# Optimization experiments

Measured on AMD Instinct MI355X. Metric: run time of the kernel, lower is better.

## Reference

```python
import jax, jax.numpy as jnp
import numpy as np

B, N_INST, H, W = 8, 64, 480, 480
EPS = 1e-12  # torch F.normalize eps


def setup_inputs() -> dict:
    key = jax.random.key(0)
    k1, k2, k3, k4, k5, k6 = jax.random.split(key, 6)
    # binary instance masks (output of connected-component labeling in the original)
    instance_masks = (jax.random.uniform(k1, (N_INST, H, W)) < 0.3).astype(jnp.float32)
    sample_ids = jax.random.randint(k2, (N_INST,), 0, B, dtype=jnp.int64)
    quaternion = jax.random.normal(k3, (B, 4, H, W), dtype=jnp.float32)
    scales = jax.random.normal(k4, (B, 3, H, W), dtype=jnp.float32)
    xy = jax.random.normal(k5, (B, 2, H, W), dtype=jnp.float32)
    z = jax.random.normal(k6, (B, H, W), dtype=jnp.float32)
    return {"instance_masks": instance_masks, "sample_ids": sample_ids,
            "quaternion": quaternion, "scales": scales, "xy": xy, "z": z}


def reference(instance_masks, sample_ids, quaternion, scales, xy, z):
    # instance_masks: [N,H,W] binary float; sample_ids: [N] in [0,B)
    mask_size = jnp.sum(instance_masks, axis=(-2, -1))  # [N]

    def masked_mean(d):  # d: [N,C,H,W] -> [N,C]
        return jnp.einsum('nhw,nchw->nc', instance_masks, d) / mask_size[:, None]

    # quaternion: masked mean then L2-normalize along channel dim
    q_agg = masked_mean(quaternion[sample_ids])                       # [N,4]
    q_agg = q_agg / jnp.maximum(jnp.linalg.norm(q_agg, axis=1, keepdims=True), EPS)
    # scales: masked mean
    s_agg = masked_mean(scales[sample_ids])                           # [N,3]
    # z: masked mean of [N,1,H,W] then exp
    z_agg = jnp.exp(masked_mean(z[sample_ids][:, None]))              # [N,1]
    # xy: masked dense map (passed on to hough voting downstream)
    xy_masked = instance_masks[:, None] * xy[sample_ids]              # [N,2,H,W]
    return q_agg, s_agg, z_agg, xy_masked
```

## Files before the change

### kernel.cpp

```cpp
#include <hip/hip_runtime.h>
#include <math.h>

#define HW      (480 * 480)
#define HW4     (HW / 4)
#define NINST   64
#define NB      8
#define NV      9
#define GI      8
#define ITER    3
#define NBLK    75
#define THREADS 256

typedef float f4 __attribute__((ext_vector_type(4)));

__device__ __forceinline__ float dot4(const float4 a, const float4 b) {
    return (a.x * b.x + a.y * b.y) + (a.z * b.z + a.w * b.w);
}

template <int CTRL>
__device__ __forceinline__ float dpp_add(float x) {
    int s = __builtin_amdgcn_update_dpp(0, __float_as_int(x), CTRL, 0xf, 0xf, false);
    return x + __int_as_float(s);
}
__device__ __forceinline__ float wave_sum(float x) {
    x = dpp_add<0x111>(x);
    x = dpp_add<0x112>(x);
    x = dpp_add<0x114>(x);
    x = dpp_add<0x118>(x);
    x = dpp_add<0x142>(x);
    x = dpp_add<0x143>(x);
    return x;
}

__global__ __launch_bounds__(THREADS, 2) void agg_main(
    const float* __restrict__ masks,
    const int*   __restrict__ sids,
    const float* __restrict__ quat,
    const float* __restrict__ scales,
    const float* __restrict__ xy,
    const float* __restrict__ z,
    float*       __restrict__ out,
    float*       __restrict__ part)
{
    const int tid = threadIdx.x;
    const int bx  = blockIdx.x;
    const int b   = blockIdx.y;

    __shared__ int   ilist[NINST];
    __shared__ int   scnt;
    __shared__ float swred[4][GI * NV];

    if (tid < 64) {
        const bool mine = (sids[tid] == b);
        const unsigned long long mk = __ballot(mine);
        if (mine) {
            const int rank = __popcll(mk & ((1ull << tid) - 1ull));
            ilist[rank] = tid;
        }
        if (tid == 0) scnt = __popcll(mk);
    }
    __syncthreads();
    const int cnt = scnt;

    const float4* M  = (const float4*)masks;
    const float4* Q  = (const float4*)quat   + (size_t)b * 4 * HW4;
    const float4* S  = (const float4*)scales + (size_t)b * 3 * HW4;
    const float4* X  = (const float4*)xy     + (size_t)b * 2 * HW4;
    const float4* Zp = (const float4*)z      + (size_t)b * HW4;
    f4*           O  = (f4*)(out + 512);

    const int lane = tid & 63;
    const int wid  = tid >> 6;

    for (int g0 = 0; g0 < cnt; g0 += GI) {
        int  nidx[GI];
        bool valid[GI];
#pragma unroll
        for (int j = 0; j < GI; ++j) {
            valid[j] = (g0 + j < cnt);
            nidx[j]  = ilist[valid[j] ? (g0 + j) : (cnt - 1)];
        }

        float acc[GI][NV];
#pragma unroll
        for (int j = 0; j < GI; ++j)
#pragma unroll
            for (int v = 0; v < NV; ++v) acc[j][v] = 0.0f;

#pragma unroll
        for (int it = 0; it < ITER; ++it) {
            const int i = (bx * ITER + it) * THREADS + tid;

            float4 m[GI];
#pragma unroll
            for (int j = 0; j < GI; ++j)
                m[j] = M[(size_t)nidx[j] * HW4 + i];
            const float4 vq0 = Q[0 * HW4 + i];
            const float4 vq1 = Q[1 * HW4 + i];
            const float4 vq2 = Q[2 * HW4 + i];
            const float4 vq3 = Q[3 * HW4 + i];
            const float4 vs0 = S[0 * HW4 + i];
            const float4 vs1 = S[1 * HW4 + i];
            const float4 vs2 = S[2 * HW4 + i];
            const float4 vx0 = X[0 * HW4 + i];
            const float4 vx1 = X[1 * HW4 + i];
            const float4 vz  = Zp[i];

#pragma unroll
            for (int j = 0; j < GI; ++j) {
                if (valid[j]) {
                    f4 o0 = { m[j].x * vx0.x, m[j].y * vx0.y,
                              m[j].z * vx0.z, m[j].w * vx0.w };
                    f4 o1 = { m[j].x * vx1.x, m[j].y * vx1.y,
                              m[j].z * vx1.z, m[j].w * vx1.w };
                    __builtin_nontemporal_store(o0, &O[((size_t)nidx[j] * 2 + 0) * HW4 + i]);
                    __builtin_nontemporal_store(o1, &O[((size_t)nidx[j] * 2 + 1) * HW4 + i]);
                }
            }

#pragma unroll
            for (int j = 0; j < GI; ++j) {
                acc[j][0] += (m[j].x + m[j].y) + (m[j].z + m[j].w);
                acc[j][1] += dot4(m[j], vq0);
                acc[j][2] += dot4(m[j], vq1);
                acc[j][3] += dot4(m[j], vq2);
                acc[j][4] += dot4(m[j], vq3);
                acc[j][5] += dot4(m[j], vs0);
                acc[j][6] += dot4(m[j], vs1);
                acc[j][7] += dot4(m[j], vs2);
                acc[j][8] += dot4(m[j], vz);
            }
        }

#pragma unroll
        for (int j = 0; j < GI; ++j)
#pragma unroll
            for (int v = 0; v < NV; ++v) {
                const float t = wave_sum(acc[j][v]);
                if (lane == 63) swred[wid][j * NV + v] = t;
            }
        __syncthreads();
        if (tid < GI * NV) {
            const int j = tid / NV;
            const int v = tid - j * NV;
            if (g0 + j < cnt) {
                const int n = ilist[g0 + j];
                part[((size_t)n * NBLK + bx) * NV + v] =
                    (swred[0][tid] + swred[1][tid]) + (swred[2][tid] + swred[3][tid]);
            }
        }
        __syncthreads();
    }
}

__global__ __launch_bounds__(THREADS) void agg_final(
    const float* __restrict__ part,
    float*       __restrict__ out)
{
    const int n   = blockIdx.x;
    const int tid = threadIdx.x;

    float vals[NV];
#pragma unroll
    for (int v = 0; v < NV; ++v) vals[v] = 0.0f;
    for (int c = tid; c < NBLK; c += THREADS) {
        const float* p = part + ((size_t)n * NBLK + c) * NV;
#pragma unroll
        for (int v = 0; v < NV; ++v) vals[v] += p[v];
    }

    __shared__ float sred[4][NV];
    const int lane = tid & 63;
    const int wid  = tid >> 6;
#pragma unroll
    for (int v = 0; v < NV; ++v) {
        float x = vals[v];
#pragma unroll
        for (int off = 32; off > 0; off >>= 1)
            x += __shfl_down(x, off, 64);
        if (lane == 0) sred[wid][v] = x;
    }
    __syncthreads();

    if (tid == 0) {
        float s[NV];
#pragma unroll
        for (int v = 0; v < NV; ++v)
            s[v] = (sred[0][v] + sred[1][v]) + (sred[2][v] + sred[3][v]);

        const float inv = 1.0f / s[0];
        const float q0 = s[1] * inv, q1 = s[2] * inv, q2 = s[3] * inv, q3 = s[4] * inv;
        const float norm = sqrtf(q0 * q0 + q1 * q1 + q2 * q2 + q3 * q3);
        const float d = fmaxf(norm, 1e-12f);
        out[n * 4 + 0] = q0 / d;
        out[n * 4 + 1] = q1 / d;
        out[n * 4 + 2] = q2 / d;
        out[n * 4 + 3] = q3 / d;

        out[256 + n * 3 + 0] = s[5] * inv;
        out[256 + n * 3 + 1] = s[6] * inv;
        out[256 + n * 3 + 2] = s[7] * inv;

        out[448 + n] = expf(s[8] * inv);
    }
}

extern "C" void kernel_launch(void* const* d_in, const int* in_sizes, int n_in,
                              void* d_out, int out_size, void* d_ws, size_t ws_size,
                              hipStream_t stream) {
    const float* masks  = (const float*)d_in[0];
    const int*   sids   = (const int*)d_in[1];
    const float* quat   = (const float*)d_in[2];
    const float* scales = (const float*)d_in[3];
    const float* xy     = (const float*)d_in[4];
    const float* z      = (const float*)d_in[5];
    float* out  = (float*)d_out;
    float* part = (float*)d_ws;

    dim3 grid(NBLK, NB);
    agg_main<<<grid, THREADS, 0, stream>>>(masks, sids, quat, scales, xy, z, out, part);
    agg_final<<<NINST, THREADS, 0, stream>>>(part, out);
}
```

Baseline: 253.1 us.

## Sort instances by batch and assign blocks to balanced instance groups

Each block now owns one group of four instances from a single batch. Blocks find their group from an in-kernel counting sort of sample ids and stride over the pixels, replacing the old scheme where each batch block serially walked all of its instances in groups of eight. The aim is to remove the load imbalance from uneven instance counts per batch and to raise occupancy by using smaller per-thread accumulators and a higher launch bound. The cost is that the dense quaternion, scale, xy and z maps are re-read by more groups. Some grid rows also exit early and do no work.

```diff
diff --git a/kernel.cpp b/kernel.cpp
--- a/kernel.cpp
+++ b/kernel.cpp
@@ -1,14 +1,13 @@
 #include <hip/hip_runtime.h>
 #include <math.h>
 
-#define HW      (480 * 480)
-#define HW4     (HW / 4)
+#define HW4     57600
 #define NINST   64
 #define NB      8
 #define NV      9
-#define GI      8
-#define ITER    3
-#define NBLK    75
+#define GI      4
+#define NQMAX   22
+#define NBLKX   90
 #define THREADS 256
 
 typedef float f4 __attribute__((ext_vector_type(4)));
@@ -32,7 +31,7 @@
     return x;
 }
 
-__global__ __launch_bounds__(THREADS, 2) void agg_main(
+__global__ __launch_bounds__(THREADS, 4) void agg_main(
     const float* __restrict__ masks,
     const int*   __restrict__ sids,
     const float* __restrict__ quat,
@@ -44,23 +43,49 @@
 {
     const int tid = threadIdx.x;
     const int bx  = blockIdx.x;
-    const int b   = blockIdx.y;
-
-    __shared__ int   ilist[NINST];
-    __shared__ int   scnt;
+    const int q   = blockIdx.y;
+
+    __shared__ int   sorted_l[NINST];
+    __shared__ int   cnt_l[NB];
     __shared__ float swred[4][GI * NV];
 
     if (tid < 64) {
-        const bool mine = (sids[tid] == b);
-        const unsigned long long mk = __ballot(mine);
-        if (mine) {
-            const int rank = __popcll(mk & ((1ull << tid) - 1ull));
-            ilist[rank] = tid;
-        }
-        if (tid == 0) scnt = __popcll(mk);
+        const int mine = sids[tid];
+        int pos = 0;
+        unsigned long long mymask = 0;
+        for (int b = 0; b < NB; ++b) {
+            const unsigned long long mb = __ballot(mine == b);
+            if (tid == 0) cnt_l[b] = __popcll(mb);
+            if (b < mine) pos += __popcll(mb);
+            if (b == mine) mymask = mb;
+        }
+        pos += __popcll(mymask & ((1ull << tid) - 1ull));
+        sorted_l[pos] = tid;
     }
     __syncthreads();
-    const int cnt = scnt;
+
+    int b = -1, qloc = 0, sstart = 0;
+    {
+        int qacc = 0, cacc = 0;
+        for (int bb = 0; bb < NB; ++bb) {
+            const int c  = cnt_l[bb];
+            const int ng = (c + GI - 1) / GI;
+            if (q >= qacc && q < qacc + ng) { b = bb; qloc = q - qacc; sstart = cacc; }
+            qacc += ng;
+            cacc += c;
+        }
+    }
+    if (b < 0) return;
+    const int cnt = cnt_l[b];
+
+    int  nidx[GI];
+    bool valid[GI];
+#pragma unroll
+    for (int j = 0; j < GI; ++j) {
+        const int l = qloc * GI + j;
+        valid[j] = (l < cnt);
+        nidx[j]  = sorted_l[sstart + (valid[j] ? l : (cnt - 1))];
+    }
 
     const float4* M  = (const float4*)masks;
     const float4* Q  = (const float4*)quat   + (size_t)b * 4 * HW4;
@@ -69,87 +94,73 @@
     const float4* Zp = (const float4*)z      + (size_t)b * HW4;
     f4*           O  = (f4*)(out + 512);
 
+    float acc[GI][NV];
+#pragma unroll
+    for (int j = 0; j < GI; ++j)
+#pragma unroll
+        for (int v = 0; v < NV; ++v) acc[j][v] = 0.0f;
+
+    for (int i = bx * THREADS + tid; i < HW4; i += NBLKX * THREADS) {
+        float4 m[GI];
+#pragma unroll
+        for (int j = 0; j < GI; ++j)
+            m[j] = M[(size_t)nidx[j] * HW4 + i];
+        const float4 vq0 = Q[0 * HW4 + i];
+        const float4 vq1 = Q[1 * HW4 + i];
+        const float4 vq2 = Q[2 * HW4 + i];
+        const float4 vq3 = Q[3 * HW4 + i];
+        const float4 vs0 = S[0 * HW4 + i];
+        const float4 vs1 = S[1 * HW4 + i];
+        const float4 vs2 = S[2 * HW4 + i];
+        const float4 vx0 = X[0 * HW4 + i];
+        const float4 vx1 = X[1 * HW4 + i];
+        const float4 vz  = Zp[i];
+
+#pragma unroll
+        for (int j = 0; j < GI; ++j) {
+            if (valid[j]) {
+                f4 o0 = { m[j].x * vx0.x, m[j].y * vx0.y,
+                          m[j].z * vx0.z, m[j].w * vx0.w };
+                f4 o1 = { m[j].x * vx1.x, m[j].y * vx1.y,
+                          m[j].z * vx1.z, m[j].w * vx1.w };
+                __builtin_nontemporal_store(o0, &O[((size_t)nidx[j] * 2 + 0) * HW4 + i]);
+                __builtin_nontemporal_store(o1, &O[((size_t)nidx[j] * 2 + 1) * HW4 + i]);
+            }
+        }
+
+#pragma unroll
+        for (int j = 0; j < GI; ++j) {
+            acc[j][0] += (m[j].x + m[j].y) + (m[j].z + m[j].w);
+            acc[j][1] += dot4(m[j], vq0);
+            acc[j][2] += dot4(m[j], vq1);
+            acc[j][3] += dot4(m[j], vq2);
+            acc[j][4] += dot4(m[j], vq3);
+            acc[j][5] += dot4(m[j], vs0);
+            acc[j][6] += dot4(m[j], vs1);
+            acc[j][7] += dot4(m[j], vs2);
+            acc[j][8] += dot4(m[j], vz);
+        }
+    }
+
     const int lane = tid & 63;
     const int wid  = tid >> 6;
-
-    for (int g0 = 0; g0 < cnt; g0 += GI) {
-        int  nidx[GI];
-        bool valid[GI];
-#pragma unroll
-        for (int j = 0; j < GI; ++j) {
-            valid[j] = (g0 + j < cnt);
-            nidx[j]  = ilist[valid[j] ? (g0 + j) : (cnt - 1)];
-        }
-
-        float acc[GI][NV];
-#pragma unroll
-        for (int j = 0; j < GI; ++j)
-#pragma unroll
-            for (int v = 0; v < NV; ++v) acc[j][v] = 0.0f;
-
-#pragma unroll
-        for (int it = 0; it < ITER; ++it) {
-            const int i = (bx * ITER + it) * THREADS + tid;
-
-            float4 m[GI];
-#pragma unroll
-            for (int j = 0; j < GI; ++j)
-                m[j] = M[(size_t)nidx[j] * HW4 + i];
-            const float4 vq0 = Q[0 * HW4 + i];
-            const float4 vq1 = Q[1 * HW4 + i];
-            const float4 vq2 = Q[2 * HW4 + i];
-            const float4 vq3 = Q[3 * HW4 + i];
-            const float4 vs0 = S[0 * HW4 + i];
-            const float4 vs1 = S[1 * HW4 + i];
-            const float4 vs2 = S[2 * HW4 + i];
-            const float4 vx0 = X[0 * HW4 + i];
-            const float4 vx1 = X[1 * HW4 + i];
-            const float4 vz  = Zp[i];
-
-#pragma unroll
-            for (int j = 0; j < GI; ++j) {
-                if (valid[j]) {
-                    f4 o0 = { m[j].x * vx0.x, m[j].y * vx0.y,
-                              m[j].z * vx0.z, m[j].w * vx0.w };
-                    f4 o1 = { m[j].x * vx1.x, m[j].y * vx1.y,
-                              m[j].z * vx1.z, m[j].w * vx1.w };
-                    __builtin_nontemporal_store(o0, &O[((size_t)nidx[j] * 2 + 0) * HW4 + i]);
-                    __builtin_nontemporal_store(o1, &O[((size_t)nidx[j] * 2 + 1) * HW4 + i]);
-                }
-            }
-
-#pragma unroll
-            for (int j = 0; j < GI; ++j) {
-                acc[j][0] += (m[j].x + m[j].y) + (m[j].z + m[j].w);
-                acc[j][1] += dot4(m[j], vq0);
-                acc[j][2] += dot4(m[j], vq1);
-                acc[j][3] += dot4(m[j], vq2);
-                acc[j][4] += dot4(m[j], vq3);
-                acc[j][5] += dot4(m[j], vs0);
-                acc[j][6] += dot4(m[j], vs1);
-                acc[j][7] += dot4(m[j], vs2);
-                acc[j][8] += dot4(m[j], vz);
-            }
-        }
-
-#pragma unroll
-        for (int j = 0; j < GI; ++j)
-#pragma unroll
-            for (int v = 0; v < NV; ++v) {
-                const float t = wave_sum(acc[j][v]);
-                if (lane == 63) swred[wid][j * NV + v] = t;
-            }
-        __syncthreads();
-        if (tid < GI * NV) {
-            const int j = tid / NV;
-            const int v = tid - j * NV;
-            if (g0 + j < cnt) {
-                const int n = ilist[g0 + j];
-                part[((size_t)n * NBLK + bx) * NV + v] =
-                    (swred[0][tid] + swred[1][tid]) + (swred[2][tid] + swred[3][tid]);
-            }
-        }
-        __syncthreads();
+#pragma unroll
+    for (int j = 0; j < GI; ++j)
+#pragma unroll
+        for (int v = 0; v < NV; ++v) {
+            const float t = wave_sum(acc[j][v]);
+            if (lane == 63) swred[wid][j * NV + v] = t;
+        }
+    __syncthreads();
+    if (tid < GI * NV) {
+        const int j = tid / NV;
+        const int v = tid - j * NV;
+        const int l = qloc * GI + j;
+        if (l < cnt) {
+            const int n = sorted_l[sstart + l];
+            part[((size_t)n * NBLKX + bx) * NV + v] =
+                (swred[0][tid] + swred[1][tid]) + (swred[2][tid] + swred[3][tid]);
+        }
     }
 }
 
@@ -163,8 +174,8 @@
     float vals[NV];
 #pragma unroll
     for (int v = 0; v < NV; ++v) vals[v] = 0.0f;
-    for (int c = tid; c < NBLK; c += THREADS) {
-        const float* p = part + ((size_t)n * NBLK + c) * NV;
+    for (int c = tid; c < NBLKX; c += THREADS) {
+        const float* p = part + ((size_t)n * NBLKX + c) * NV;
 #pragma unroll
         for (int v = 0; v < NV; ++v) vals[v] += p[v];
     }
@@ -217,7 +228,7 @@
     float* out  = (float*)d_out;
     float* part = (float*)d_ws;
 
-    dim3 grid(NBLK, NB);
+    dim3 grid(NBLKX, NQMAX);
     agg_main<<<grid, THREADS, 0, stream>>>(masks, sids, quat, scales, xy, z, out, part);
     agg_final<<<NINST, THREADS, 0, stream>>>(part, out);
 }
```

After: 249.1 us. Within noise of the previous version (-1.6%).
